# Optimization experiments

Hardware: AMD Instinct MI355X
Metric: run time of the kernel (lower is better)

## Reference

```python
import jax, jax.numpy as jnp
import numpy as np

N, E, FD, H, NG, LAT = 20000, 320000, 64, 4, 64, 512


def _gat(x, W, a_src, a_dst, b, src, dst):
    # x: [N, in]; W: [H*FD, in]; a_src/a_dst: [H, FD]; b: [H*FD]
    h = (x @ W.T).reshape(N, H, FD)
    s = jnp.sum(h * a_src, -1)   # [N, H]
    d = jnp.sum(h * a_dst, -1)   # [N, H]
    e = jax.nn.leaky_relu(s[src] + d[dst], negative_slope=0.2)  # [E', H]
    m = jax.ops.segment_max(e, dst, num_segments=N)
    ex = jnp.exp(e - m[dst])
    den = jax.ops.segment_sum(ex, dst, num_segments=N)
    alpha = ex / den[dst]                                        # [E', H]
    out = jax.ops.segment_sum(alpha[:, :, None] * h[src], dst, num_segments=N)
    return out.reshape(N, H * FD) + b


def setup_inputs() -> dict:
    key = jax.random.key(0)
    ks = jax.random.split(key, 24)
    inp = {}
    inp['street_feature'] = jax.random.normal(ks[0], (N, 128), jnp.float32)
    inp['building_feature'] = jax.random.normal(ks[1], (N, 5), jnp.float32)
    sm = jax.random.randint(ks[2], (N, 1), 0, 2).astype(jnp.float32)
    inp['street_mask'] = sm
    inp['building_mask'] = 1.0 - sm
    inp['edge_index'] = jax.random.randint(ks[3], (2, E), 0, N, dtype=jnp.int32)
    # batch: sorted graph ids covering all NG graphs (no empty segments)
    rest = jax.random.randint(ks[4], (N - NG,), 0, NG, dtype=jnp.int32)
    inp['batch'] = jnp.sort(jnp.concatenate([jnp.arange(NG, dtype=jnp.int32), rest]))

    def lin(k, o, i):
        s = 1.0 / np.sqrt(i)
        return jax.random.uniform(k, (o, i), jnp.float32, -s, s)

    inp['street_W'] = lin(ks[5], FD, 128); inp['street_b'] = jnp.zeros((FD,), jnp.float32)
    inp['building_W'] = lin(ks[6], FD, 5); inp['building_b'] = jnp.zeros((FD,), jnp.float32)
    inp['W1'] = lin(ks[7], H * FD, FD)
    inp['a_src1'] = jax.random.normal(ks[8], (H, FD), jnp.float32) * 0.1
    inp['a_dst1'] = jax.random.normal(ks[9], (H, FD), jnp.float32) * 0.1
    inp['b1'] = jnp.zeros((H * FD,), jnp.float32)
    inp['W2'] = lin(ks[10], H * FD, H * FD)
    inp['a_src2'] = jax.random.normal(ks[11], (H, FD), jnp.float32) * 0.1
    inp['a_dst2'] = jax.random.normal(ks[12], (H, FD), jnp.float32) * 0.1
    inp['b2'] = jnp.zeros((H * FD,), jnp.float32)
    inp['W3'] = lin(ks[13], H * FD, H * FD)
    inp['a_src3'] = jax.random.normal(ks[14], (H, FD), jnp.float32) * 0.1
    inp['a_dst3'] = jax.random.normal(ks[15], (H, FD), jnp.float32) * 0.1
    inp['b3'] = jnp.zeros((H * FD,), jnp.float32)
    agg_in = FD * (1 + H * 3)  # 832
    inp['agg_W'] = lin(ks[16], LAT, agg_in); inp['agg_b'] = jnp.zeros((LAT,), jnp.float32)
    inp['mu_W'] = lin(ks[17], LAT, LAT); inp['mu_b'] = jnp.zeros((LAT,), jnp.float32)
    inp['var_W'] = lin(ks[18], LAT, LAT); inp['var_b'] = jnp.zeros((LAT,), jnp.float32)
    return inp


def reference(street_feature, building_feature, street_mask, building_mask,
              edge_index, batch,
              street_W, street_b, building_W, building_b,
              W1, a_src1, a_dst1, b1, W2, a_src2, a_dst2, b2,
              W3, a_src3, a_dst3, b3, agg_W, agg_b, mu_W, mu_b, var_W, var_b):
    sf = jax.nn.relu(street_feature @ street_W.T + street_b)
    bf = jax.nn.relu(building_feature @ building_W.T + building_b)
    n0 = sf * street_mask + bf * building_mask  # [N, FD]
    # add self loops (PyG GATConv default)
    loop = jnp.arange(N, dtype=edge_index.dtype)
    src = jnp.concatenate([edge_index[0], loop])
    dst = jnp.concatenate([edge_index[1], loop])
    n1 = jax.nn.relu(_gat(n0, W1, a_src1, a_dst1, b1, src, dst))
    n2 = jax.nn.relu(_gat(n1, W2, a_src2, a_dst2, b2, src, dst))
    n3 = jax.nn.relu(_gat(n2, W3, a_src3, a_dst3, b3, src, dst))
    g0 = jax.ops.segment_max(n0, batch, num_segments=NG)
    g1 = jax.ops.segment_max(n1, batch, num_segments=NG)
    g2 = jax.ops.segment_max(n2, batch, num_segments=NG)
    g3 = jax.ops.segment_max(n3, batch, num_segments=NG)
    g = jnp.concatenate([g0, g1, g2, g3], axis=1)  # [NG, FD*(1+3H)]
    latent = g @ agg_W.T + agg_b
    mu = latent @ mu_W.T + mu_b
    log_var = latent @ var_W.T + var_b
    return (mu, log_var)
```

## Files before the change

### kernel.cpp

```cpp
#include <hip/hip_runtime.h>
#include <math.h>

#define NNODES 20000
#define NEDGES 320000
#define FDIM 64
#define NHEAD 4
#define NGR 64
#define LATD 512
#define HF 256
#define NEP (NEDGES + NNODES)
#define AGGIN 832
#define MPAD 20032

#define EDGE_BLOCKS4 ((NEP + 1023) / 1024)
#define CONV_N (HF * FDIM + 2 * HF * HF)
#define CONV_BLOCKS ((CONV_N + 255) / 256)
#define ENC_BLOCKS (NNODES / 32)
#define GEMM_BLOCKS (NNODES / 32)
#define SLAB_BLOCKS (NNODES / 32)
#define AGGR_BLOCKS (NNODES / 4)

typedef float f32x4 __attribute__((ext_vector_type(4)));
typedef _Float16 f16x8 __attribute__((ext_vector_type(8)));
typedef unsigned short u16x8 __attribute__((ext_vector_type(8)));

__device__ inline unsigned short f2h(float f) {
    _Float16 h = (_Float16)f;
    unsigned short u;
    __builtin_memcpy(&u, &h, 2);
    return u;
}
__device__ inline float h2f(unsigned short u) {
    _Float16 h;
    __builtin_memcpy(&h, &u, 2);
    return (float)h;
}

struct MegaParams {
    const float *sfeat, *bfeat, *smask, *bmask;
    const int *ei, *batch;
    const float *sW, *sb, *bW, *bb;
    const float *W1, *as1, *ad1, *b1;
    const float *W2, *as2, *ad2, *b2;
    const float *W3, *as3, *ad3, *b3;
    const float *aggW, *aggb, *muW, *mub, *vW, *varb;
    float *out;
    unsigned short *h, *x0, *xA, *W1f, *W2f, *W3f;
    float *s, *d, *g, *lat;
    int *offs, *cnt, *cnt2, *csr, *gi;
};


__device__ __forceinline__ void count_body(int vb, int t,
    const int* __restrict__ ei, int* __restrict__ cnt)
{
    int i0 = vb * 1024 + t;
#pragma unroll
    for (int u = 0; u < 4; u++) {
        int i = i0 + u * 256;
        if (i < NEDGES) {
            atomicAdd(&cnt[ei[NEDGES + i]], 1);
        } else if (i < NEP) {
            atomicAdd(&cnt[i - NEDGES], 1);
        }
    }
}

__device__ __forceinline__ void convert_body(int vb, int t,
    const float* __restrict__ W1, const float* __restrict__ W2, const float* __restrict__ W3,
    unsigned short* __restrict__ W1f, unsigned short* __restrict__ W2f,
    unsigned short* __restrict__ W3f)
{
    int i = vb * 256 + t;
    const int n1 = HF * FDIM, n2 = HF * HF;
    const float* src; unsigned short* dst; int j;
    if (i < n1) { src = W1; dst = W1f; j = i; }
    else if (i < n1 + n2) { src = W2; dst = W2f; j = i - n1; }
    else if (i < n1 + 2 * n2) { src = W3; dst = W3f; j = i - n1 - n2; }
    else return;
    dst[j] = f2h(src[j]);
}

__device__ __forceinline__ void encode_body(int venc, int t, float* wlds, float* xlds,
    const float* __restrict__ sfeat, const float* __restrict__ bfeat,
    const float* __restrict__ smask, const float* __restrict__ bmask,
    const float* __restrict__ sW, const float* __restrict__ sb,
    const float* __restrict__ bW, const float* __restrict__ bb,
    const int* __restrict__ batch,
    unsigned short* __restrict__ x0, int* __restrict__ g)
{
#pragma unroll
    for (int it = 0; it < 8; it++) {
        int idx = it * 256 + t;
        int f = idx >> 5, k4 = idx & 31;
        float4 v = *(const float4*)(sW + f * 128 + k4 * 4);
        *(float4*)(&wlds[f * 132 + k4 * 4]) = v;
    }
    int nb0 = venc * 32;
#pragma unroll
    for (int it = 0; it < 4; it++) {
        int idx = it * 256 + t;
        int node = idx >> 5, k4 = idx & 31;
        float4 v = *(const float4*)(sfeat + (size_t)(nb0 + node) * 128 + k4 * 4);
        *(float4*)(&xlds[node * 132 + k4 * 4]) = v;
    }
    __syncthreads();

    int lane = t & 63, wave = t >> 6;
    int nb = nb0 + wave * 8;

    float acc[8];
#pragma unroll
    for (int i = 0; i < 8; i++) acc[i] = 0.f;

    for (int k4 = 0; k4 < 32; k4++) {
        float4 wv = *(const float4*)(&wlds[lane * 132 + k4 * 4]);
#pragma unroll
        for (int i = 0; i < 8; i++) {
            float4 xv = *(const float4*)(&xlds[(wave * 8 + i) * 132 + k4 * 4]);
            acc[i] += xv.x * wv.x + xv.y * wv.y + xv.z * wv.z + xv.w * wv.w;
        }
    }

    float bwr[5];
#pragma unroll
    for (int k = 0; k < 5; k++) bwr[k] = bW[lane * 5 + k];
    float sbv = sb[lane], bbv = bb[lane];

    int curb = batch[nb];
    float m = 0.f;
#pragma unroll
    for (int i = 0; i < 8; i++) {
        int node = nb + i;
        float accb = 0.f;
#pragma unroll
        for (int k = 0; k < 5; k++) accb += bfeat[node * 5 + k] * bwr[k];
        float sv = fmaxf(acc[i] + sbv, 0.f);
        float bv = fmaxf(accb + bbv, 0.f);
        float val = sv * smask[node] + bv * bmask[node];
        x0[(size_t)node * FDIM + lane] = f2h(val);
        int b = batch[node];
        if (b != curb) {
            atomicMax(&g[curb * AGGIN + lane], __float_as_int(m));
            m = 0.f; curb = b;
        }
        m = fmaxf(m, val);
    }
    atomicMax(&g[curb * AGGIN + lane], __float_as_int(m));
}

__device__ __forceinline__ void scatter_body(int vb, int t,
    const int* __restrict__ ei, const int* __restrict__ offs,
    int* __restrict__ cnt2, int* __restrict__ csr_src)
{
    int i0 = vb * 1024 + t;
    int sv[4], dv[4];
#pragma unroll
    for (int u = 0; u < 4; u++) {
        int i = i0 + u * 256;
        if (i < NEDGES) { sv[u] = ei[i]; dv[u] = ei[NEDGES + i]; }
        else if (i < NEP) { sv[u] = i - NEDGES; dv[u] = i - NEDGES; }
        else { sv[u] = -1; dv[u] = 0; }
    }
#pragma unroll
    for (int u = 0; u < 4; u++) {
        if (sv[u] >= 0) {
            int p = offs[dv[u]] + atomicAdd(&cnt2[dv[u]], 1);
            csr_src[p] = sv[u];
        }
    }
}

template <int K>
__device__ __forceinline__ void gemm_body(int vbg, int t,
    const unsigned short* __restrict__ xf, const unsigned short* __restrict__ Wf,
    const float* __restrict__ a_src, const float* __restrict__ a_dst,
    unsigned short* __restrict__ h, float* __restrict__ s, float* __restrict__ d)
{
    constexpr int NCHUNK = K / 64;
    int lane = t & 63, w = t >> 6;
    int colid = lane & 15, quad = lane >> 4;
    int nb = vbg * 32;

    f32x4 acc[2][4];
#pragma unroll
    for (int mt = 0; mt < 2; mt++)
#pragma unroll
        for (int nt = 0; nt < 4; nt++)
#pragma unroll
            for (int r = 0; r < 4; r++) acc[mt][nt][r] = 0.f;

#pragma unroll
    for (int c = 0; c < NCHUNK; c++) {
        const int kc = c * 64;
        f16x8 ah[2][2], bh[4][2];
#pragma unroll
        for (int half = 0; half < 2; half++) {
#pragma unroll
            for (int mt = 0; mt < 2; mt++) {
                size_t aoff = (size_t)(nb + mt * 16 + colid) * K + kc + half * 32 + quad * 8;
                ah[mt][half] = *(const f16x8*)&xf[aoff];
            }
#pragma unroll
            for (int nt = 0; nt < 4; nt++) {
                size_t boff = (size_t)(w * 64 + nt * 16 + colid) * K + kc + half * 32 + quad * 8;
                bh[nt][half] = *(const f16x8*)&Wf[boff];
            }
        }
        __builtin_amdgcn_sched_barrier(0);
#pragma unroll
        for (int half = 0; half < 2; half++)
#pragma unroll
            for (int mt = 0; mt < 2; mt++)
#pragma unroll
                for (int nt = 0; nt < 4; nt++)
                    acc[mt][nt] = __builtin_amdgcn_mfma_f32_16x16x32_f16(ah[mt][half], bh[nt][half], acc[mt][nt], 0, 0, 0);
    }

#pragma unroll
    for (int mt = 0; mt < 2; mt++) {
#pragma unroll
        for (int r = 0; r < 4; r++) {
            int node = nb + mt * 16 + quad * 4 + r;
#pragma unroll
            for (int nt = 0; nt < 4; nt++)
                h[(size_t)node * HF + w * 64 + nt * 16 + colid] = f2h(acc[mt][nt][r]);
        }
    }

    float as_r[4], ad_r[4];
#pragma unroll
    for (int nt = 0; nt < 4; nt++) {
        as_r[nt] = a_src[w * 64 + nt * 16 + colid];
        ad_r[nt] = a_dst[w * 64 + nt * 16 + colid];
    }
#pragma unroll
    for (int mt = 0; mt < 2; mt++) {
#pragma unroll
        for (int r = 0; r < 4; r++) {
            float ps = 0.f, pd = 0.f;
#pragma unroll
            for (int nt = 0; nt < 4; nt++) {
                ps += acc[mt][nt][r] * as_r[nt];
                pd += acc[mt][nt][r] * ad_r[nt];
            }
#pragma unroll
            for (int m = 1; m < 16; m <<= 1) {
                ps += __shfl_xor(ps, m, 64);
                pd += __shfl_xor(pd, m, 64);
            }
            if (colid == 0) {
                int node = nb + mt * 16 + quad * 4 + r;
                s[(size_t)node * NHEAD + w] = ps;
                d[(size_t)node * NHEAD + w] = pd;
            }
        }
    }
}

__device__ __forceinline__ void aggr_body(int vba, int t,
    const unsigned short* __restrict__ h, const float* __restrict__ s, const float* __restrict__ d,
    const int* __restrict__ offs, const int* __restrict__ csr_src,
    const float* __restrict__ bias, unsigned short* __restrict__ out)
{
    int lane = t & 63;
    int wv = t >> 6;
    int node = vba * 4 + wv;
    int eh = lane >> 5;
    int p = lane & 31;
    int hd2 = p >> 3;
    int f0 = p * 8;
    int lo = offs[node], hi = offs[node + 1];
    int deg = hi - lo;

    float a[8];
#pragma unroll
    for (int j = 0; j < 8; j++) a[j] = 0.f;
    float inv;

    if (deg <= 64) {
        int slot = lane >> 2, hd = lane & 3;
        float dn = d[(size_t)node * NHEAD + hd];
        float ev[4];
        int sv[4];
#pragma unroll
        for (int c = 0; c < 4; c++) {
            int k = c * 16 + slot;
            float e = -3.402823466e38f;
            int src = 0;
            if (k < deg) {
                src = csr_src[lo + k];
                float ee = s[(size_t)src * NHEAD + hd] + dn;
                e = fmaxf(ee, 0.2f * ee);
            }
            ev[c] = e; sv[c] = src;
        }
        float mx = fmaxf(fmaxf(ev[0], ev[1]), fmaxf(ev[2], ev[3]));
#pragma unroll
        for (int m = 4; m < 64; m <<= 1) mx = fmaxf(mx, __shfl_xor(mx, m, 64));
        float den = 0.f;
#pragma unroll
        for (int c = 0; c < 4; c++) {
            ev[c] = __expf(ev[c] - mx);
            den += ev[c];
        }
#pragma unroll
        for (int m = 4; m < 64; m <<= 1) den += __shfl_xor(den, m, 64);

        inv = 1.f / __shfl(den, hd2);

#pragma unroll
        for (int cb = 0; cb < 2; cb++) {
            if (cb * 32 >= deg) break;
            float ex[16]; int sr[16]; u16x8 hv[16];
#pragma unroll
            for (int cc = 0; cc < 2; cc++) {
                int c = cb * 2 + cc;
#pragma unroll
                for (int u = 0; u < 8; u++) {
                    int sl = (u * 2 + eh) * 4 + hd2;
                    ex[cc * 8 + u] = __shfl(ev[c], sl);
                    sr[cc * 8 + u] = __shfl(sv[c], sl);
                }
            }
#pragma unroll
            for (int u = 0; u < 16; u++)
                hv[u] = *(const u16x8*)(h + (size_t)sr[u] * HF + f0);
#pragma unroll
            for (int u = 0; u < 16; u++)
#pragma unroll
                for (int j = 0; j < 8; j++) a[j] += ex[u] * h2f(hv[u][j]);
        }
    } else {
        float dn2 = d[(size_t)node * NHEAD + hd2];
        float mx = -3.402823466e38f;
        for (int i = lo; i < hi; i++) {
            int src = csr_src[i];
            float e = s[(size_t)src * NHEAD + hd2] + dn2;
            e = fmaxf(e, 0.2f * e);
            mx = fmaxf(mx, e);
        }
        float den = 0.f;
        for (int i = lo + eh; i < hi; i += 2) {
            int src = csr_src[i];
            float e = s[(size_t)src * NHEAD + hd2] + dn2;
            e = fmaxf(e, 0.2f * e);
            float ex = __expf(e - mx);
            den += ex;
            u16x8 hv = *(const u16x8*)(h + (size_t)src * HF + f0);
#pragma unroll
            for (int j = 0; j < 8; j++) a[j] += ex * h2f(hv[j]);
        }
        den += __shfl_xor(den, 32, 64);
        inv = 1.f / den;
    }

#pragma unroll
    for (int j = 0; j < 8; j++) a[j] += __shfl_xor(a[j], 32, 64);

    if (eh == 0) {
        u16x8 ov;
#pragma unroll
        for (int j = 0; j < 8; j++)
            ov[j] = f2h(fmaxf(a[j] * inv + bias[f0 + j], 0.f));
        *(u16x8*)(out + (size_t)node * HF + f0) = ov;
    }
}

__device__ __forceinline__ void slab_body(int vbs, int t,
    const unsigned short* __restrict__ x, const int* __restrict__ batch,
    int* __restrict__ g, int coloff)
{
    int f = t;
    int r0 = vbs * 32;
    int cur = batch[r0];
    float m = 0.f;
    for (int r = r0; r < r0 + 32; r += 4) {
        float v[4]; int bb[4];
#pragma unroll
        for (int i = 0; i < 4; i++) {
            v[i] = h2f(x[(size_t)(r + i) * HF + f]);
            bb[i] = batch[r + i];
        }
#pragma unroll
        for (int i = 0; i < 4; i++) {
            if (bb[i] != cur) {
                atomicMax(&g[cur * AGGIN + coloff + f], __float_as_int(m));
                m = 0.f; cur = bb[i];
            }
            m = fmaxf(m, v[i]);
        }
    }
    atomicMax(&g[cur * AGGIN + coloff + f], __float_as_int(m));
}


__global__ __launch_bounds__(256) void k_prep_enc(MegaParams P)
{
    __shared__ float wlds[64 * 132];
    __shared__ float xlds[32 * 132];
    if ((int)blockIdx.x < EDGE_BLOCKS4)
        count_body(blockIdx.x, threadIdx.x, P.ei, P.cnt);
    else if ((int)blockIdx.x < EDGE_BLOCKS4 + CONV_BLOCKS)
        convert_body(blockIdx.x - EDGE_BLOCKS4, threadIdx.x, P.W1, P.W2, P.W3,
                     P.W1f, P.W2f, P.W3f);
    else
        encode_body(blockIdx.x - (EDGE_BLOCKS4 + CONV_BLOCKS), threadIdx.x, wlds, xlds,
                    P.sfeat, P.bfeat, P.smask, P.bmask, P.sW, P.sb, P.bW, P.bb,
                    P.batch, P.x0, P.gi);
}

__global__ __launch_bounds__(1024) void k_scan(MegaParams P)
{
    const int* deg = P.cnt;
    int* offs = P.offs;
    __shared__ int wt[16];
    const int per = (NNODES + 1023) / 1024;
    int t = threadIdx.x, lane = t & 63, w = t >> 6;
    int start = t * per;
    int end = start + per; if (end > NNODES) end = NNODES;
    int s = 0;
    for (int i = start; i < end; i++) s += deg[i];
    int pref = s;
#pragma unroll
    for (int m = 1; m < 64; m <<= 1) {
        int v = __shfl_up(pref, m, 64);
        if (lane >= m) pref += v;
    }
    if (lane == 63) wt[w] = pref;
    __syncthreads();
    int wadd = 0;
    for (int i = 0; i < w; i++) wadd += wt[i];
    int acc = wadd + pref - s;
    for (int i = start; i < end; i++) { offs[i] = acc; acc += deg[i]; }
    if (t == 1023) offs[NNODES] = NEP;
}

template <int K>
__global__ __launch_bounds__(256, 2) void k_gemm(MegaParams P,
    const unsigned short* xf, const unsigned short* Wf,
    const float* a_src, const float* a_dst, int slabcol)
{
    if ((int)blockIdx.x >= GEMM_BLOCKS) {
        if (slabcol >= 0)
            slab_body(blockIdx.x - GEMM_BLOCKS, threadIdx.x, xf, P.batch, P.gi, slabcol);
        else
            scatter_body(blockIdx.x - GEMM_BLOCKS, threadIdx.x, P.ei, P.offs, P.cnt2, P.csr);
        return;
    }
    gemm_body<K>(blockIdx.x, threadIdx.x, xf, Wf, a_src, a_dst, P.h, P.s, P.d);
}

__global__ __launch_bounds__(256) void k_aggr(MegaParams P, const float* bias)
{
    aggr_body(blockIdx.x, threadIdx.x, P.h, P.s, P.d, P.offs, P.csr, bias, P.xA);
}

__global__ __launch_bounds__(256) void k_slab(MegaParams P, int coloff)
{
    slab_body(blockIdx.x, threadIdx.x, P.xA, P.batch, P.gi, coloff);
}

__global__ __launch_bounds__(256) void k_latent(MegaParams P)
{
    int idx = blockIdx.x * 256 + threadIdx.x;
    int r = idx >> 9, c = idx & 511;
    const float4* gv = (const float4*)(P.g + (size_t)r * AGGIN);
    const float4* wv = (const float4*)(P.aggW + (size_t)c * AGGIN);
    float acc = 0.f;
#pragma unroll 4
    for (int k = 0; k < AGGIN / 4; k++) {
        float4 a = gv[k], w = wv[k];
        acc += a.x * w.x + a.y * w.y + a.z * w.z + a.w * w.w;
    }
    P.lat[idx] = acc + P.aggb[c];
}

__global__ __launch_bounds__(256) void k_head(MegaParams P)
{
    int idx = blockIdx.x * 256 + threadIdx.x;
    int half = idx >> 15;
    int j = idx & 32767;
    int r = j >> 9, c = j & 511;
    const float* W = half ? P.vW : P.muW;
    const float* bb = half ? P.varb : P.mub;
    const float4* lv = (const float4*)(P.lat + (size_t)r * LATD);
    const float4* wv = (const float4*)(W + (size_t)c * LATD);
    float acc = 0.f;
#pragma unroll 4
    for (int k = 0; k < LATD / 4; k++) {
        float4 a = lv[k], w = wv[k];
        acc += a.x * w.x + a.y * w.y + a.z * w.z + a.w * w.w;
    }
    P.out[idx] = acc + bb[c];
}

static inline size_t align16(size_t x) { return (x + 15) & ~(size_t)15; }

extern "C" void kernel_launch(void* const* d_in, const int* in_sizes, int n_in,
                              void* d_out, int out_size, void* d_ws, size_t ws_size,
                              hipStream_t stream)
{
    MegaParams P;
    P.sfeat = (const float*)d_in[0];
    P.bfeat = (const float*)d_in[1];
    P.smask = (const float*)d_in[2];
    P.bmask = (const float*)d_in[3];
    P.ei    = (const int*)d_in[4];
    P.batch = (const int*)d_in[5];
    P.sW = (const float*)d_in[6];
    P.sb = (const float*)d_in[7];
    P.bW = (const float*)d_in[8];
    P.bb = (const float*)d_in[9];
    P.W1 = (const float*)d_in[10];
    P.as1 = (const float*)d_in[11];
    P.ad1 = (const float*)d_in[12];
    P.b1 = (const float*)d_in[13];
    P.W2 = (const float*)d_in[14];
    P.as2 = (const float*)d_in[15];
    P.ad2 = (const float*)d_in[16];
    P.b2 = (const float*)d_in[17];
    P.W3 = (const float*)d_in[18];
    P.as3 = (const float*)d_in[19];
    P.ad3 = (const float*)d_in[20];
    P.b3 = (const float*)d_in[21];
    P.aggW = (const float*)d_in[22];
    P.aggb = (const float*)d_in[23];
    P.muW = (const float*)d_in[24];
    P.mub = (const float*)d_in[25];
    P.vW = (const float*)d_in[26];
    P.varb = (const float*)d_in[27];
    P.out = (float*)d_out;

    char* ws = (char*)d_ws;
    size_t off = 0;
    P.h  = (unsigned short*)(ws + off); off = align16(off + (size_t)NNODES * HF * 2);
    P.x0 = (unsigned short*)(ws + off); off = align16(off + (size_t)MPAD * FDIM * 2);
    P.xA = (unsigned short*)(ws + off); off = align16(off + (size_t)MPAD * HF * 2);
    P.s  = (float*)(ws + off); off = align16(off + (size_t)NNODES * NHEAD * 4);
    P.d  = (float*)(ws + off); off = align16(off + (size_t)NNODES * NHEAD * 4);
    P.offs = (int*)(ws + off); off = align16(off + (size_t)(NNODES + 1) * 4);
    size_t zstart = off;
    P.cnt  = (int*)(ws + off); off = align16(off + (size_t)NNODES * 4);
    P.cnt2 = (int*)(ws + off); off = align16(off + (size_t)NNODES * 4);
    P.g    = (float*)(ws + off); off = align16(off + (size_t)NGR * AGGIN * 4);
    size_t zbytes = off - zstart;
    P.csr = (int*)(ws + off); off = align16(off + (size_t)NEP * 4);
    P.lat = (float*)(ws + off); off = align16(off + (size_t)NGR * LATD * 4);
    P.W1f = (unsigned short*)(ws + off); off = align16(off + (size_t)HF * FDIM * 2);
    P.W2f = (unsigned short*)(ws + off); off = align16(off + (size_t)HF * HF * 2);
    P.W3f = (unsigned short*)(ws + off); off = align16(off + (size_t)HF * HF * 2);

    P.gi = (int*)P.g;

    hipMemsetAsync(ws + zstart, 0, zbytes, stream);

    k_prep_enc<<<EDGE_BLOCKS4 + CONV_BLOCKS + ENC_BLOCKS, 256, 0, stream>>>(P);
    k_scan<<<1, 1024, 0, stream>>>(P);

    k_gemm<FDIM><<<GEMM_BLOCKS + EDGE_BLOCKS4, 256, 0, stream>>>(P, P.x0, P.W1f, P.as1, P.ad1, -1);
    k_aggr<<<AGGR_BLOCKS, 256, 0, stream>>>(P, P.b1);

    k_gemm<HF><<<GEMM_BLOCKS + SLAB_BLOCKS, 256, 0, stream>>>(P, P.xA, P.W2f, P.as2, P.ad2, FDIM);
    k_aggr<<<AGGR_BLOCKS, 256, 0, stream>>>(P, P.b2);

    k_gemm<HF><<<GEMM_BLOCKS + SLAB_BLOCKS, 256, 0, stream>>>(P, P.xA, P.W3f, P.as3, P.ad3, FDIM + HF);
    k_aggr<<<AGGR_BLOCKS, 256, 0, stream>>>(P, P.b3);

    k_slab<<<SLAB_BLOCKS, 256, 0, stream>>>(P, FDIM + 2 * HF);
    k_latent<<<(NGR * LATD) / 256, 256, 0, stream>>>(P);
    k_head<<<(2 * NGR * LATD) / 256, 256, 0, stream>>>(P);
}
```

Measured before the change: 365.7 us.

## Precompose head weights with aggregation weights to fuse latent and head GEMMs

Precomputes Wf = [muW; vW] @ aggW and the matching composed biases in extra blocks of the prep kernel, so the tail runs one kernel computing g @ Wf^T instead of separate latent and head kernels. This removes a kernel launch and the dependent latent pass at the end of the graph, and moves the weight composition into the prep kernel where it runs alongside the edge counting and encoding. It adds a 1024x512x832 GEMM of weight-only work per call and changes the floating-point summation order. The path falls back to the old kernels if the workspace is too small.

```diff
diff --git a/kernel.cpp b/kernel.cpp
--- a/kernel.cpp
+++ b/kernel.cpp
@@ -16,6 +16,8 @@
 #define CONV_N (HF * FDIM + 2 * HF * HF)
 #define CONV_BLOCKS ((CONV_N + 255) / 256)
 #define ENC_BLOCKS (NNODES / 32)
+#define FW_BLOCKS (2 * 8 * 13)
+#define FWB_BLOCKS 4
 #define GEMM_BLOCKS (NNODES / 32)
 #define SLAB_BLOCKS (NNODES / 32)
 #define AGGR_BLOCKS (NNODES / 4)
@@ -46,8 +48,9 @@
     const float *aggW, *aggb, *muW, *mub, *vW, *varb;
     float *out;
     unsigned short *h, *x0, *xA, *W1f, *W2f, *W3f;
-    float *s, *d, *g, *lat;
+    float *s, *d, *g, *lat, *Wf, *bf;
     int *offs, *cnt, *cnt2, *csr, *gi;
+    int fused;
 };
 
 
@@ -149,6 +152,75 @@
     atomicMax(&g[curb * AGGIN + lane], __float_as_int(m));
 }
 
+__device__ __forceinline__ void fw_body(int vb, int t, float* lds,
+    const float* __restrict__ muW, const float* __restrict__ vW,
+    const float* __restrict__ aggW, float* __restrict__ Wf)
+{
+    float* As = lds;
+    float* Bs = lds + 64 * 68;
+    int head = vb / 104, rem = vb % 104;
+    int ct = rem / 13, jt = rem % 13;
+    int c0 = ct * 64, j0 = jt * 64;
+    const float* M = head ? vW : muW;
+    int ty = t >> 4, tx = t & 15;
+
+    float acc[4][4];
+#pragma unroll
+    for (int a = 0; a < 4; a++)
+#pragma unroll
+        for (int b = 0; b < 4; b++) acc[a][b] = 0.f;
+
+    for (int kt = 0; kt < 8; kt++) {
+        int k0 = kt * 64;
+#pragma unroll
+        for (int it = 0; it < 4; it++) {
+            int idx = it * 256 + t;
+            int row = idx >> 4, c4 = (idx & 15) * 4;
+            *(float4*)&As[row * 68 + c4] = *(const float4*)&M[(size_t)(c0 + row) * 512 + k0 + c4];
+            *(float4*)&Bs[row * 68 + c4] = *(const float4*)&aggW[(size_t)(k0 + row) * 832 + j0 + c4];
+        }
+        __syncthreads();
+#pragma unroll 4
+        for (int kk = 0; kk < 64; kk++) {
+            float a0 = As[(ty * 4 + 0) * 68 + kk];
+            float a1 = As[(ty * 4 + 1) * 68 + kk];
+            float a2 = As[(ty * 4 + 2) * 68 + kk];
+            float a3 = As[(ty * 4 + 3) * 68 + kk];
+            float4 b4 = *(const float4*)&Bs[kk * 68 + tx * 4];
+            acc[0][0] += a0 * b4.x; acc[0][1] += a0 * b4.y; acc[0][2] += a0 * b4.z; acc[0][3] += a0 * b4.w;
+            acc[1][0] += a1 * b4.x; acc[1][1] += a1 * b4.y; acc[1][2] += a1 * b4.z; acc[1][3] += a1 * b4.w;
+            acc[2][0] += a2 * b4.x; acc[2][1] += a2 * b4.y; acc[2][2] += a2 * b4.z; acc[2][3] += a2 * b4.w;
+            acc[3][0] += a3 * b4.x; acc[3][1] += a3 * b4.y; acc[3][2] += a3 * b4.z; acc[3][3] += a3 * b4.w;
+        }
+        __syncthreads();
+    }
+#pragma unroll
+    for (int a = 0; a < 4; a++) {
+        float4 v; v.x = acc[a][0]; v.y = acc[a][1]; v.z = acc[a][2]; v.w = acc[a][3];
+        *(float4*)&Wf[((size_t)(head * 512) + c0 + ty * 4 + a) * 832 + j0 + tx * 4] = v;
+    }
+}
+
+__device__ __forceinline__ void fwbias_body(int vb, int t,
+    const float* __restrict__ muW, const float* __restrict__ mub,
+    const float* __restrict__ vW, const float* __restrict__ varb,
+    const float* __restrict__ aggb, float* __restrict__ bf)
+{
+    int idx = vb * 256 + t;
+    int head = idx >> 9, c = idx & 511;
+    const float* M = head ? vW : muW;
+    const float* base = head ? varb : mub;
+    const float4* mv = (const float4*)(M + (size_t)c * 512);
+    const float4* av = (const float4*)aggb;
+    float acc = 0.f;
+#pragma unroll 4
+    for (int k = 0; k < 512 / 4; k++) {
+        float4 a = mv[k], b = av[k];
+        acc += a.x * b.x + a.y * b.y + a.z * b.z + a.w * b.w;
+    }
+    bf[idx] = acc + base[c];
+}
+
 __device__ __forceinline__ void scatter_body(int vb, int t,
     const int* __restrict__ ei, const int* __restrict__ offs,
     int* __restrict__ cnt2, int* __restrict__ csr_src)
@@ -397,17 +469,27 @@
 
 __global__ __launch_bounds__(256) void k_prep_enc(MegaParams P)
 {
-    __shared__ float wlds[64 * 132];
-    __shared__ float xlds[32 * 132];
-    if ((int)blockIdx.x < EDGE_BLOCKS4)
-        count_body(blockIdx.x, threadIdx.x, P.ei, P.cnt);
-    else if ((int)blockIdx.x < EDGE_BLOCKS4 + CONV_BLOCKS)
-        convert_body(blockIdx.x - EDGE_BLOCKS4, threadIdx.x, P.W1, P.W2, P.W3,
+    __shared__ char smem[96 * 132 * 4];
+    int b = blockIdx.x;
+    if (b < EDGE_BLOCKS4) {
+        count_body(b, threadIdx.x, P.ei, P.cnt);
+    } else if (b < EDGE_BLOCKS4 + CONV_BLOCKS) {
+        convert_body(b - EDGE_BLOCKS4, threadIdx.x, P.W1, P.W2, P.W3,
                      P.W1f, P.W2f, P.W3f);
-    else
-        encode_body(blockIdx.x - (EDGE_BLOCKS4 + CONV_BLOCKS), threadIdx.x, wlds, xlds,
+    } else if (b < EDGE_BLOCKS4 + CONV_BLOCKS + ENC_BLOCKS) {
+        float* wlds = (float*)smem;
+        float* xlds = wlds + 64 * 132;
+        encode_body(b - (EDGE_BLOCKS4 + CONV_BLOCKS), threadIdx.x, wlds, xlds,
                     P.sfeat, P.bfeat, P.smask, P.bmask, P.sW, P.sb, P.bW, P.bb,
                     P.batch, P.x0, P.gi);
+    } else if (P.fused) {
+        int fb = b - (EDGE_BLOCKS4 + CONV_BLOCKS + ENC_BLOCKS);
+        if (fb < FW_BLOCKS)
+            fw_body(fb, threadIdx.x, (float*)smem, P.muW, P.vW, P.aggW, P.Wf);
+        else
+            fwbias_body(fb - FW_BLOCKS, threadIdx.x, P.muW, P.mub, P.vW, P.varb,
+                        P.aggb, P.bf);
+    }
 }
 
 __global__ __launch_bounds__(1024) void k_scan(MegaParams P)
@@ -459,6 +541,23 @@
 __global__ __launch_bounds__(256) void k_slab(MegaParams P, int coloff)
 {
     slab_body(blockIdx.x, threadIdx.x, P.xA, P.batch, P.gi, coloff);
+}
+
+__global__ __launch_bounds__(256) void k_head_fused(MegaParams P)
+{
+    int idx = blockIdx.x * 256 + threadIdx.x;
+    int half = idx >> 15;
+    int j = idx & 32767;
+    int r = j >> 9, c = j & 511;
+    const float4* gv = (const float4*)(P.g + (size_t)r * AGGIN);
+    const float4* wv = (const float4*)(P.Wf + ((size_t)(half * 512) + c) * 832);
+    float acc = 0.f;
+#pragma unroll 4
+    for (int k = 0; k < AGGIN / 4; k++) {
+        float4 a = gv[k], w = wv[k];
+        acc += a.x * w.x + a.y * w.y + a.z * w.z + a.w * w.w;
+    }
+    P.out[idx] = acc + P.bf[half * 512 + c];
 }
 
 __global__ __launch_bounds__(256) void k_latent(MegaParams P)
@@ -550,12 +649,17 @@
     P.W1f = (unsigned short*)(ws + off); off = align16(off + (size_t)HF * FDIM * 2);
     P.W2f = (unsigned short*)(ws + off); off = align16(off + (size_t)HF * HF * 2);
     P.W3f = (unsigned short*)(ws + off); off = align16(off + (size_t)HF * HF * 2);
+    P.Wf = (float*)(ws + off); off = align16(off + (size_t)2 * 512 * 832 * 4);
+    P.bf = (float*)(ws + off); off = align16(off + (size_t)2 * 512 * 4);
+    P.fused = (off <= ws_size) ? 1 : 0;
 
     P.gi = (int*)P.g;
 
     hipMemsetAsync(ws + zstart, 0, zbytes, stream);
 
-    k_prep_enc<<<EDGE_BLOCKS4 + CONV_BLOCKS + ENC_BLOCKS, 256, 0, stream>>>(P);
+    int prep_blocks = EDGE_BLOCKS4 + CONV_BLOCKS + ENC_BLOCKS
+                    + (P.fused ? (FW_BLOCKS + FWB_BLOCKS) : 0);
+    k_prep_enc<<<prep_blocks, 256, 0, stream>>>(P);
     k_scan<<<1, 1024, 0, stream>>>(P);
 
     k_gemm<FDIM><<<GEMM_BLOCKS + EDGE_BLOCKS4, 256, 0, stream>>>(P, P.x0, P.W1f, P.as1, P.ad1, -1);
@@ -568,6 +672,11 @@
     k_aggr<<<AGGR_BLOCKS, 256, 0, stream>>>(P, P.b3);
 
     k_slab<<<SLAB_BLOCKS, 256, 0, stream>>>(P, FDIM + 2 * HF);
-    k_latent<<<(NGR * LATD) / 256, 256, 0, stream>>>(P);
-    k_head<<<(2 * NGR * LATD) / 256, 256, 0, stream>>>(P);
-}
+
+    if (P.fused) {
+        k_head_fused<<<(2 * NGR * LATD) / 256, 256, 0, stream>>>(P);
+    } else {
+        k_latent<<<(NGR * LATD) / 256, 256, 0, stream>>>(P);
+        k_head<<<(2 * NGR * LATD) / 256, 256, 0, stream>>>(P);
+    }
+}
```

New measurement: 364.0 us. About the same (-0.5%).
